# Performance work log

Hardware: AMD Instinct MI355X
Metric: run time of the kernel (lower is better)

The kernel has to match this reference:

```python
import jax, jax.numpy as jnp
import numpy as np

EMBED_DIM = 256


def setup_inputs() -> dict:
    key = jax.random.key(0)
    k1, k2, k3 = jax.random.split(key, 3)
    B, S, E = 4, 256, EMBED_DIM
    component_repr = jax.random.normal(k1, (B, S, E), dtype=jnp.float32)
    # nn.Linear(2E, E): weight [E, 2E], bias [E]
    bound = 1.0 / np.sqrt(2 * E)
    W = jax.random.uniform(k2, (E, 2 * E), minval=-bound, maxval=bound, dtype=jnp.float32)
    b = jax.random.uniform(k3, (E,), minval=-bound, maxval=bound, dtype=jnp.float32)
    return {"component_repr": component_repr, "W": W, "b": b}


def reference(component_repr, W, b):
    # Faithful to: cat([comp_i, comp_j], -1) @ W.T + b
    # Split W into halves acting on comp_i and comp_j; avoids the [B,S,S,2E] concat.
    E = component_repr.shape[-1]
    W1, W2 = W[:, :E], W[:, E:]
    pi = jnp.einsum('bse,fe->bsf', component_repr, W1)  # [B,S,E]
    pj = jnp.einsum('bse,fe->bsf', component_repr, W2)  # [B,S,E]
    # broadcast to pairwise [B,S,S,E]
    return pi[:, :, None, :] + pj[:, None, :, :] + b
```

## Files before the change

### kernel.cpp

```cpp
#include <hip/hip_runtime.h>

typedef __attribute__((ext_vector_type(4))) float float4v;

__global__ __launch_bounds__(256) void gemm_pipj(
    const float* __restrict__ x, const float* __restrict__ W,
    const float* __restrict__ bias,
    float* __restrict__ pib, float* __restrict__ pj) {
    const int r0 = blockIdx.x * 4;
    const int f = threadIdx.x;
    __shared__ float xs[4][256];
#pragma unroll
    for (int k = 0; k < 4; ++k)
        xs[k][f] = x[(size_t)(r0 + k) * 256 + f];
    __syncthreads();

    const float4v* wr = (const float4v*)(W + (size_t)f * 512);
    float acc0[4] = {0.f, 0.f, 0.f, 0.f};
    float acc1[4] = {0.f, 0.f, 0.f, 0.f};
#pragma unroll 4
    for (int e4 = 0; e4 < 64; ++e4) {
        float4v w1 = wr[e4];
        float4v w2 = wr[e4 + 64];
#pragma unroll
        for (int r = 0; r < 4; ++r) {
            float x0 = xs[r][e4 * 4 + 0];
            float x1 = xs[r][e4 * 4 + 1];
            float x2 = xs[r][e4 * 4 + 2];
            float x3 = xs[r][e4 * 4 + 3];
            acc0[r] += x0 * w1.x + x1 * w1.y + x2 * w1.z + x3 * w1.w;
            acc1[r] += x0 * w2.x + x1 * w2.y + x2 * w2.z + x3 * w2.w;
        }
    }
    float bv = bias[f];
#pragma unroll
    for (int r = 0; r < 4; ++r) {
        pib[(size_t)(r0 + r) * 256 + f] = acc0[r] + bv;
        pj [(size_t)(r0 + r) * 256 + f] = acc1[r];
    }
}

__global__ __launch_bounds__(256) void bcast_add(
    const float* __restrict__ pib, const float* __restrict__ pj,
    float* __restrict__ out) {
    const int bi   = blockIdx.x >> 1;
    const int half = blockIdx.x & 1;
    const int t = threadIdx.x;
    const int w = t >> 6;
    const int f0 = (t & 63) * 4;
    const int b = bi >> 8;
    const int j0 = half * 128 + w * 32;

    const float4v a = *(const float4v*)(pib + (size_t)bi * 256 + f0);
    const float* pjbase = pj + ((size_t)(b * 256 + j0)) * 256 + f0;
    float* obase = out + (((size_t)bi * 256) + j0) * 256 + f0;
#pragma unroll 8
    for (int jj = 0; jj < 32; ++jj) {
        float4v p = *(const float4v*)(pjbase + (size_t)jj * 256);
        float4v v = a + p;
        __builtin_nontemporal_store(v, (float4v*)(obase + (size_t)jj * 256));
    }
}

extern "C" void kernel_launch(void* const* d_in, const int* in_sizes, int n_in,
                              void* d_out, int out_size, void* d_ws, size_t ws_size,
                              hipStream_t stream) {
    const float* x    = (const float*)d_in[0];
    const float* W    = (const float*)d_in[1];
    const float* bias = (const float*)d_in[2];
    float* out = (float*)d_out;

    float* pib = (float*)d_ws;
    float* pj  = pib + 1024 * 256;

    gemm_pipj<<<256, 256, 0, stream>>>(x, W, bias, pib, pj);
    bcast_add<<<2048, 256, 0, stream>>>(pib, pj, out);
}
```

Measured before the change: 284.5 us.

## Transpose W so GEMM loads coalesce, and use plain stores in broadcast

Adds a kernel that transposes W into workspace so the projection GEMM can read weights with coalesced float4 loads across threads. Each thread now computes four output features for one row instead of one feature for four rows. The broadcast kernel's nontemporal stores become regular stores. The cost is an extra kernel launch and a W round-trip through memory. The output write (256MB-scale) still dominates, and dropping the nontemporal hint may change cache behaviour on that write.

```diff
diff --git a/kernel.cpp b/kernel.cpp
--- a/kernel.cpp
+++ b/kernel.cpp
@@ -2,41 +2,50 @@
 
 typedef __attribute__((ext_vector_type(4))) float float4v;
 
+__global__ __launch_bounds__(256) void transposeW(
+    const float* __restrict__ W, float* __restrict__ Wt) {
+    __shared__ float tile[64][65];
+    const int ta = blockIdx.x & 3;
+    const int tc = blockIdx.x >> 2;
+    const int lx = threadIdx.x & 63;
+    const int ly = threadIdx.x >> 6;
+#pragma unroll
+    for (int rr = 0; rr < 64; rr += 4)
+        tile[rr + ly][lx] = W[(size_t)(ta * 64 + rr + ly) * 512 + tc * 64 + lx];
+    __syncthreads();
+#pragma unroll
+    for (int rr = 0; rr < 64; rr += 4)
+        Wt[(size_t)(tc * 64 + rr + ly) * 256 + ta * 64 + lx] = tile[lx][rr + ly];
+}
+
 __global__ __launch_bounds__(256) void gemm_pipj(
-    const float* __restrict__ x, const float* __restrict__ W,
+    const float* __restrict__ x, const float* __restrict__ Wt,
     const float* __restrict__ bias,
     float* __restrict__ pib, float* __restrict__ pj) {
     const int r0 = blockIdx.x * 4;
-    const int f = threadIdx.x;
+    const int t = threadIdx.x;
+    const int rw = t >> 6;
+    const int fq = t & 63;
     __shared__ float xs[4][256];
 #pragma unroll
     for (int k = 0; k < 4; ++k)
-        xs[k][f] = x[(size_t)(r0 + k) * 256 + f];
+        ((float*)xs)[k * 256 + t] = x[(size_t)r0 * 256 + k * 256 + t];
     __syncthreads();
 
-    const float4v* wr = (const float4v*)(W + (size_t)f * 512);
-    float acc0[4] = {0.f, 0.f, 0.f, 0.f};
-    float acc1[4] = {0.f, 0.f, 0.f, 0.f};
+    const float4v* wt = (const float4v*)Wt;
+    float4v acc0 = {0.f, 0.f, 0.f, 0.f};
+    float4v acc1 = {0.f, 0.f, 0.f, 0.f};
 #pragma unroll 4
-    for (int e4 = 0; e4 < 64; ++e4) {
-        float4v w1 = wr[e4];
-        float4v w2 = wr[e4 + 64];
-#pragma unroll
-        for (int r = 0; r < 4; ++r) {
-            float x0 = xs[r][e4 * 4 + 0];
-            float x1 = xs[r][e4 * 4 + 1];
-            float x2 = xs[r][e4 * 4 + 2];
-            float x3 = xs[r][e4 * 4 + 3];
-            acc0[r] += x0 * w1.x + x1 * w1.y + x2 * w1.z + x3 * w1.w;
-            acc1[r] += x0 * w2.x + x1 * w2.y + x2 * w2.z + x3 * w2.w;
-        }
+    for (int e = 0; e < 256; ++e) {
+        float xv = xs[rw][e];
+        float4v w1 = wt[(size_t)e * 64 + fq];
+        float4v w2 = wt[(size_t)(e + 256) * 64 + fq];
+        acc0 += w1 * xv;
+        acc1 += w2 * xv;
     }
-    float bv = bias[f];
-#pragma unroll
-    for (int r = 0; r < 4; ++r) {
-        pib[(size_t)(r0 + r) * 256 + f] = acc0[r] + bv;
-        pj [(size_t)(r0 + r) * 256 + f] = acc1[r];
-    }
+    const float4v bv = *(const float4v*)(bias + fq * 4);
+    *(float4v*)(pib + (size_t)(r0 + rw) * 256 + fq * 4) = acc0 + bv;
+    *(float4v*)(pj  + (size_t)(r0 + rw) * 256 + fq * 4) = acc1;
 }
 
 __global__ __launch_bounds__(256) void bcast_add(
@@ -56,8 +65,7 @@
 #pragma unroll 8
     for (int jj = 0; jj < 32; ++jj) {
         float4v p = *(const float4v*)(pjbase + (size_t)jj * 256);
-        float4v v = a + p;
-        __builtin_nontemporal_store(v, (float4v*)(obase + (size_t)jj * 256));
+        *(float4v*)(obase + (size_t)jj * 256) = a + p;
     }
 }
 
@@ -71,7 +79,9 @@
 
     float* pib = (float*)d_ws;
     float* pj  = pib + 1024 * 256;
+    float* Wt  = pj  + 1024 * 256;
 
-    gemm_pipj<<<256, 256, 0, stream>>>(x, W, bias, pib, pj);
+    transposeW<<<32, 256, 0, stream>>>(W, Wt);
+    gemm_pipj<<<256, 256, 0, stream>>>(x, Wt, bias, pib, pj);
     bcast_add<<<2048, 256, 0, stream>>>(pib, pj, out);
 }
```

Result: no change. 280.2 us (-1.5%).
